# Kernel optimization log

Hardware: AMD Instinct MI355X
Metric: run time of the kernel (lower is better)

The kernel has to match this reference:

```python
import jax, jax.numpy as jnp
import numpy as np

N = 1024
D = 128          # node_dim
NUM_LAYERS = 3
H_CLS = 128      # edge classifier hidden


def setup_inputs() -> dict:
    key = jax.random.key(0)
    ks = jax.random.split(key, 20)
    s_in = 1.0 / np.sqrt(3.0)
    s_d = 1.0 / np.sqrt(D)
    s_2d = 1.0 / np.sqrt(2 * D)
    s_h = 1.0 / np.sqrt(H_CLS)
    inp = {
        "node_features": jax.random.uniform(ks[0], (N, 3), jnp.float32),
        "adj_matrix": jax.random.uniform(ks[1], (N, N), jnp.float32),
        "edge_weights": jax.random.normal(ks[2], (N, N, 1), jnp.float32),
        # node embedding Linear(3, D)
        "W_embed": jax.random.uniform(ks[3], (3, D), jnp.float32, -s_in, s_in),
        "b_embed": jax.random.uniform(ks[4], (D,), jnp.float32, -s_in, s_in),
        # stacked GCN layer params, [L, ...]
        "Wu": jax.random.uniform(ks[5], (NUM_LAYERS, D, D), jnp.float32, -s_d, s_d),
        "bu": jax.random.uniform(ks[6], (NUM_LAYERS, D), jnp.float32, -s_d, s_d),
        "Wv": jax.random.uniform(ks[7], (NUM_LAYERS, D, D), jnp.float32, -s_d, s_d),
        "bv": jax.random.uniform(ks[8], (NUM_LAYERS, D), jnp.float32, -s_d, s_d),
        "Wg": jax.random.uniform(ks[9], (NUM_LAYERS, 2 * D, D), jnp.float32, -s_2d, s_2d),
        "bg": jax.random.uniform(ks[10], (NUM_LAYERS, D), jnp.float32, -s_2d, s_2d),
        # edge classifier: Linear(2D, 128) -> ReLU -> Linear(128, 1)
        "Wc1": jax.random.uniform(ks[11], (2 * D, H_CLS), jnp.float32, -s_2d, s_2d),
        "bc1": jax.random.uniform(ks[12], (H_CLS,), jnp.float32, -s_2d, s_2d),
        "Wc2": jax.random.uniform(ks[13], (H_CLS, 1), jnp.float32, -s_h, s_h),
        "bc2": jax.random.uniform(ks[14], (1,), jnp.float32, -s_h, s_h),
    }
    return inp


def reference(node_features, adj_matrix, edge_weights,
              W_embed, b_embed, Wu, bu, Wv, bv, Wg, bg,
              Wc1, bc1, Wc2, bc2):
    h = node_features @ W_embed + b_embed                       # [N, D]
    for l in range(NUM_LAYERS):
        u = h @ Wu[l] + bu[l]                                   # [N, D]
        v = h @ Wv[l] + bv[l]                                   # [N, D]
        agg = adj_matrix @ v                                    # [N, D]
        # gate Linear(2D, D) on cat([u, agg]) == u @ Wg[:D] + agg @ Wg[D:]
        gate = jax.nn.sigmoid(u @ Wg[l, :D] + agg @ Wg[l, D:] + bg[l])
        h = jax.nn.relu(h + gate * agg)
    # edge classifier: cat([h_i, h_j]) @ Wc1 == (h @ Wc1[:D])[i] + (h @ Wc1[D:])[j]
    hi = h @ Wc1[:D]                                            # [N, H]
    hj = h @ Wc1[D:]                                            # [N, H]
    hidden = jax.nn.relu(hi[:, None, :] + hj[None, :, :] + bc1) # [N, N, H]
    logits = jnp.einsum('ijh,h->ij', hidden, Wc2[:, 0]) + bc2[0]  # [N, N]
    loss = jnp.mean(jnp.square(logits * adj_matrix - edge_weights[..., 0]))
    return logits, loss
```

## Files before the change

kernel.cpp:

```cpp
#include <hip/hip_runtime.h>

#define NN 1024
#define DD 128
#define NBLK 256

typedef __attribute__((ext_vector_type(4))) float f32x4;

__device__ __forceinline__ void scstore(float* p, float v) {
    __hip_atomic_store((unsigned*)p, __float_as_uint(v),
                       __ATOMIC_RELAXED, __HIP_MEMORY_SCOPE_AGENT);
}

__device__ __forceinline__ void gridbar(unsigned* bar, unsigned ep) {
    __syncthreads();
    if (threadIdx.x == 0) {
        asm volatile("s_waitcnt vmcnt(0)" ::: "memory");
        unsigned old = __hip_atomic_fetch_add(&bar[(blockIdx.x & 15) << 5], 1u,
                                              __ATOMIC_RELAXED, __HIP_MEMORY_SCOPE_AGENT);
        if (old == (ep << 4) - 1) {
            unsigned mold = __hip_atomic_fetch_add(&bar[512], 1u,
                                                   __ATOMIC_RELAXED, __HIP_MEMORY_SCOPE_AGENT);
            if (mold == (ep << 4) - 1)
                __hip_atomic_store(&bar[544], ep, __ATOMIC_RELAXED, __HIP_MEMORY_SCOPE_AGENT);
        }
        while (__hip_atomic_load(&bar[544], __ATOMIC_RELAXED, __HIP_MEMORY_SCOPE_AGENT) < ep)
            __builtin_amdgcn_s_sleep(4);
    }
    __syncthreads();
}

__device__ __forceinline__ float dotW2(const float* __restrict__ W, const float* x, int d) {
    float a0 = 0.f, a1 = 0.f;
#pragma unroll 2
    for (int k = 0; k < DD; k += 8) {
        f32x4 xa = *(const f32x4*)(x + k);
        f32x4 xb = *(const f32x4*)(x + k + 4);
        a0 = fmaf(xa[0], W[(k + 0) * DD + d], a0);
        a0 = fmaf(xa[1], W[(k + 1) * DD + d], a0);
        a0 = fmaf(xa[2], W[(k + 2) * DD + d], a0);
        a0 = fmaf(xa[3], W[(k + 3) * DD + d], a0);
        a1 = fmaf(xb[0], W[(k + 4) * DD + d], a1);
        a1 = fmaf(xb[1], W[(k + 5) * DD + d], a1);
        a1 = fmaf(xb[2], W[(k + 6) * DD + d], a1);
        a1 = fmaf(xb[3], W[(k + 7) * DD + d], a1);
    }
    return a0 + a1;
}

__global__ __launch_bounds__(1024, 4) void k_fused(
    const float* __restrict__ adj, const float* __restrict__ ew,
    const float* __restrict__ nf, const float* __restrict__ We, const float* __restrict__ be,
    const float* __restrict__ Wu, const float* __restrict__ bu,
    const float* __restrict__ Wv, const float* __restrict__ bv,
    const float* __restrict__ Wg, const float* __restrict__ bg,
    const float* __restrict__ Wc1, const float* __restrict__ bc1,
    const float* __restrict__ Wc2, const float* __restrict__ bc2,
    float* __restrict__ vA, float* __restrict__ vB, float* __restrict__ vC,
    float* __restrict__ hi, float* __restrict__ hj,
    float* __restrict__ S1, float* __restrict__ S2,
    float* __restrict__ lossAcc, unsigned* __restrict__ counter,
    unsigned* __restrict__ barCnt, float* __restrict__ outL)
{
    __shared__ float hS[4][DD], uS[4][DD], aggS[4][DD];
    __shared__ float gg[2][4][DD];
    __shared__ float sred[2][4][2];
    __shared__ float wS[DD];
    __shared__ union {
        struct { float adjS[4][NN]; float pS[16][4][DD]; } g;
        struct { float hiS[64][132]; float hjS[64][130]; float lred[16]; } e;
    } sm;

    int tid = threadIdx.x, bx = blockIdx.x;
    int row0 = bx * 4;
    int halfq = tid >> 9, rq = (tid >> 7) & 3, d = tid & 127;
    unsigned ep = 0;

    {
        int r = tid >> 8, k0 = (tid & 255) << 2;
        *(f32x4*)&sm.g.adjS[r][k0] = *(const f32x4*)(adj + (size_t)(row0 + r) * NN + k0);
    }
    if (tid < 512) {
        int r = tid >> 7;
        float a = be[d];
#pragma unroll
        for (int k = 0; k < 3; ++k) a = fmaf(nf[(row0 + r) * 3 + k], We[k * DD + d], a);
        hS[r][d] = a;
    }
    __syncthreads();
    {
        float acc = dotW2(halfq ? Wv : Wu, hS[rq], d);
        if (!halfq) uS[rq][d] = acc + bu[d];
        else        scstore(&vA[(size_t)(row0 + rq) * DD + d], acc + bv[d]);
    }
    gridbar(barCnt, ++ep);

    for (int l = 0; l < 3; ++l) {
        const float* vin = (l == 0) ? vA : (l == 1) ? vB : vC;
        float* vout = (l == 0) ? vB : vC;

        {
            int kk = tid >> 5, dq = tid & 31;
            int d0 = dq << 2, kb = kk << 5;
            f32x4 ac0 = {0.f,0.f,0.f,0.f}, ac1 = ac0, ac2 = ac0, ac3 = ac0;
#pragma unroll 2
            for (int ku = 0; ku < 32; ku += 4) {
                f32x4 a0 = *(const f32x4*)&sm.g.adjS[0][kb + ku];
                f32x4 a1 = *(const f32x4*)&sm.g.adjS[1][kb + ku];
                f32x4 a2 = *(const f32x4*)&sm.g.adjS[2][kb + ku];
                f32x4 a3 = *(const f32x4*)&sm.g.adjS[3][kb + ku];
#pragma unroll
                for (int j = 0; j < 4; ++j) {
                    f32x4 v4 = *(const f32x4*)(vin + (size_t)(kb + ku + j) * DD + d0);
#pragma unroll
                    for (int c = 0; c < 4; ++c) {
                        ac0[c] = fmaf(a0[j], v4[c], ac0[c]);
                        ac1[c] = fmaf(a1[j], v4[c], ac1[c]);
                        ac2[c] = fmaf(a2[j], v4[c], ac2[c]);
                        ac3[c] = fmaf(a3[j], v4[c], ac3[c]);
                    }
                }
            }
            if (kk >= 16) {
                int ks = kk - 16;
                *(f32x4*)&sm.g.pS[ks][0][d0] = ac0;
                *(f32x4*)&sm.g.pS[ks][1][d0] = ac1;
                *(f32x4*)&sm.g.pS[ks][2][d0] = ac2;
                *(f32x4*)&sm.g.pS[ks][3][d0] = ac3;
            }
            __syncthreads();
            if (kk < 16) {
                f32x4 p0 = *(const f32x4*)&sm.g.pS[kk][0][d0];
                f32x4 p1 = *(const f32x4*)&sm.g.pS[kk][1][d0];
                f32x4 p2 = *(const f32x4*)&sm.g.pS[kk][2][d0];
                f32x4 p3 = *(const f32x4*)&sm.g.pS[kk][3][d0];
#pragma unroll
                for (int c = 0; c < 4; ++c) {
                    p0[c] += ac0[c]; p1[c] += ac1[c]; p2[c] += ac2[c]; p3[c] += ac3[c];
                }
                *(f32x4*)&sm.g.pS[kk][0][d0] = p0;
                *(f32x4*)&sm.g.pS[kk][1][d0] = p1;
                *(f32x4*)&sm.g.pS[kk][2][d0] = p2;
                *(f32x4*)&sm.g.pS[kk][3][d0] = p3;
            }
        }
        __syncthreads();
        if (tid < 512) {
            int r = tid >> 7;
            float s = 0.f;
#pragma unroll
            for (int c = 0; c < 16; ++c) s += sm.g.pS[c][r][d];
            aggS[r][d] = s;
        }
        __syncthreads();
        {
            const float* W = Wg + l * (2 * DD * DD) + (halfq ? DD * DD : 0);
            gg[halfq][rq][d] = dotW2(W, halfq ? aggS[rq] : uS[rq], d);
        }
        __syncthreads();
        if (tid < 512) {
            int r = tid >> 7;
            float g = 1.f / (1.f + __expf(-(gg[0][r][d] + gg[1][r][d] + bg[l * DD + d])));
            float nh = fmaf(g, aggS[r][d], hS[r][d]);
            hS[r][d] = nh > 0.f ? nh : 0.f;
        }
        __syncthreads();
        {
            const float* W2 = (l < 2) ? ((halfq ? Wv : Wu) + (l + 1) * DD * DD)
                                      : (Wc1 + (halfq ? DD * DD : 0));
            float acc = dotW2(W2, hS[rq], d);
            if (l < 2) {
                if (!halfq) uS[rq][d] = acc + bu[(l + 1) * DD + d];
                else        scstore(&vout[(size_t)(row0 + rq) * DD + d], acc + bv[(l + 1) * DD + d]);
            } else {
                float val = acc + (halfq ? 0.f : bc1[d]);
                scstore(&(halfq ? hj : hi)[(size_t)(row0 + rq) * DD + d], val);
                float p = val * Wc2[d];
#pragma unroll
                for (int off = 32; off; off >>= 1) p += __shfl_down(p, off);
                if ((tid & 63) == 0) sred[halfq][rq][(tid >> 6) & 1] = p;
            }
        }
        if (l == 2) {
            __syncthreads();
            if (tid < 4) scstore(&S1[row0 + tid], sred[0][tid][0] + sred[0][tid][1]);
            else if (tid < 8) scstore(&S2[row0 + tid - 4], sred[1][tid - 4][0] + sred[1][tid - 4][1]);
        }
        gridbar(barCnt, ++ep);
    }

    {
        int i0 = (bx >> 4) << 6, j0 = (bx & 15) << 6;
        if (tid < 128) wS[tid] = Wc2[tid];
        for (int e2 = tid; e2 < 2048; e2 += 1024) {
            int r = e2 >> 5, c = (e2 & 31) << 2;
            *(f32x4*)&sm.e.hiS[r][c] = *(const f32x4*)(hi + (size_t)(i0 + r) * DD + c);
            f32x4 jv = *(const f32x4*)(hj + (size_t)(j0 + r) * DD + c);
            float2 j01; j01.x = jv[0]; j01.y = jv[1];
            float2 j23; j23.x = jv[2]; j23.y = jv[3];
            *(float2*)&sm.e.hjS[r][c] = j01;
            *(float2*)&sm.e.hjS[r][c + 2] = j23;
        }
        __syncthreads();
        int ty = tid >> 5, tx = tid & 31;
        float a00 = 0.f, a01 = 0.f, a10 = 0.f, a11 = 0.f;
#pragma unroll 4
        for (int hh = 0; hh < DD; hh += 4) {
            f32x4 x0 = *(const f32x4*)&sm.e.hiS[ty][hh];
            f32x4 x1 = *(const f32x4*)&sm.e.hiS[ty + 32][hh];
            float2 y0a = *(const float2*)&sm.e.hjS[tx][hh];
            float2 y0b = *(const float2*)&sm.e.hjS[tx][hh + 2];
            float2 y1a = *(const float2*)&sm.e.hjS[tx + 32][hh];
            float2 y1b = *(const float2*)&sm.e.hjS[tx + 32][hh + 2];
            f32x4 w4 = *(const f32x4*)&wS[hh];
            a00 = fmaf(fabsf(x0[0] + y0a.x), w4[0], a00);
            a00 = fmaf(fabsf(x0[1] + y0a.y), w4[1], a00);
            a00 = fmaf(fabsf(x0[2] + y0b.x), w4[2], a00);
            a00 = fmaf(fabsf(x0[3] + y0b.y), w4[3], a00);
            a01 = fmaf(fabsf(x0[0] + y1a.x), w4[0], a01);
            a01 = fmaf(fabsf(x0[1] + y1a.y), w4[1], a01);
            a01 = fmaf(fabsf(x0[2] + y1b.x), w4[2], a01);
            a01 = fmaf(fabsf(x0[3] + y1b.y), w4[3], a01);
            a10 = fmaf(fabsf(x1[0] + y0a.x), w4[0], a10);
            a10 = fmaf(fabsf(x1[1] + y0a.y), w4[1], a10);
            a10 = fmaf(fabsf(x1[2] + y0b.x), w4[2], a10);
            a10 = fmaf(fabsf(x1[3] + y0b.y), w4[3], a10);
            a11 = fmaf(fabsf(x1[0] + y1a.x), w4[0], a11);
            a11 = fmaf(fabsf(x1[1] + y1a.y), w4[1], a11);
            a11 = fmaf(fabsf(x1[2] + y1b.x), w4[2], a11);
            a11 = fmaf(fabsf(x1[3] + y1b.y), w4[3], a11);
        }
        float bcv = bc2[0];
        int ia = i0 + ty, ib = ia + 32, ja = j0 + tx, jb = ja + 32;
        float s1a = S1[ia], s1b = S1[ib];
        float s2a = S2[ja], s2b = S2[jb];
        float lg00 = fmaf(0.5f, a00 + s1a + s2a, bcv);
        float lg01 = fmaf(0.5f, a01 + s1a + s2b, bcv);
        float lg10 = fmaf(0.5f, a10 + s1b + s2a, bcv);
        float lg11 = fmaf(0.5f, a11 + s1b + s2b, bcv);
        size_t o00 = (size_t)ia * NN + ja, o01 = (size_t)ia * NN + jb;
        size_t o10 = (size_t)ib * NN + ja, o11 = (size_t)ib * NN + jb;
        outL[o00] = lg00; outL[o01] = lg01; outL[o10] = lg10; outL[o11] = lg11;
        float t0 = fmaf(lg00, adj[o00], -ew[o00]);
        float t1 = fmaf(lg01, adj[o01], -ew[o01]);
        float t2 = fmaf(lg10, adj[o10], -ew[o10]);
        float t3 = fmaf(lg11, adj[o11], -ew[o11]);
        float ls = fmaf(t0, t0, fmaf(t1, t1, fmaf(t2, t2, t3 * t3)));
#pragma unroll
        for (int off = 32; off; off >>= 1) ls += __shfl_down(ls, off);
        if ((tid & 63) == 0) sm.e.lred[tid >> 6] = ls;
        __syncthreads();
        if (tid == 0) {
            float bls = 0.f;
#pragma unroll
            for (int w = 0; w < 16; ++w) bls += sm.e.lred[w];
            atomicAdd(lossAcc, bls);
            asm volatile("s_waitcnt vmcnt(0)" ::: "memory");
            unsigned old = atomicAdd(counter, 1u);
            if (old == NBLK - 1u) {
                unsigned Lb = __hip_atomic_load((unsigned*)lossAcc,
                                                __ATOMIC_RELAXED, __HIP_MEMORY_SCOPE_AGENT);
                outL[(size_t)NN * NN] = __uint_as_float(Lb) * (1.f / (1024.f * 1024.f));
            }
        }
    }
}

extern "C" void kernel_launch(void* const* d_in, const int* in_sizes, int n_in,
                              void* d_out, int out_size, void* d_ws, size_t ws_size,
                              hipStream_t stream)
{
    const float* nf  = (const float*)d_in[0];
    const float* adj = (const float*)d_in[1];
    const float* ew  = (const float*)d_in[2];
    const float* We  = (const float*)d_in[3];
    const float* be  = (const float*)d_in[4];
    const float* Wu  = (const float*)d_in[5];
    const float* bu  = (const float*)d_in[6];
    const float* Wv  = (const float*)d_in[7];
    const float* bv  = (const float*)d_in[8];
    const float* Wg  = (const float*)d_in[9];
    const float* bg  = (const float*)d_in[10];
    const float* Wc1 = (const float*)d_in[11];
    const float* bc1 = (const float*)d_in[12];
    const float* Wc2 = (const float*)d_in[13];
    const float* bc2 = (const float*)d_in[14];

    float* ws = (float*)d_ws;
    float* vA  = ws;
    float* vB  = ws + 131072;
    float* vC  = ws + 262144;
    float* hi  = ws + 393216;
    float* hj  = ws + 524288;
    float* S1  = ws + 655360;
    float* S2  = ws + 656384;
    float* lossAcc = ws + 657408;
    unsigned* counter = (unsigned*)(ws + 657409);
    unsigned* barCnt = (unsigned*)(ws + 657440);

    hipMemsetAsync((void*)lossAcc, 0, 2560, stream);
    k_fused<<<NBLK, 1024, 0, stream>>>(adj, ew, nf, We, be, Wu, bu, Wv, bv, Wg, bg,
                                       Wc1, bc1, Wc2, bc2, vA, vB, vC, hi, hj, S1, S2,
                                       lossAcc, counter, barCnt, (float*)d_out);
}
```

Before: 172.3 us.

## Overlap gate u-projection with adjacency aggregation via warp specialization

The block is split so the lower 512 threads compute the gate's u @ Wg[:D] product while the upper 512 threads compute the adj @ v aggregation, each covering twice the K range. This removes one barrier and the two-stage partial-sum reduction, and shortens the later gate phase to only the agg half. The cost is that the aggregation now runs on half the threads with longer per-thread loops, so the two halves may be unbalanced.

New measurement: 173.2 us. About the same (+0.5%).

```diff
diff --git a/kernel.cpp b/kernel.cpp
--- a/kernel.cpp
+++ b/kernel.cpp
@@ -98,50 +98,40 @@
         const float* vin = (l == 0) ? vA : (l == 1) ? vB : vC;
         float* vout = (l == 0) ? vB : vC;
 
-        {
-            int kk = tid >> 5, dq = tid & 31;
-            int d0 = dq << 2, kb = kk << 5;
+        if (tid < 512) {
+            const float* WA = Wg + l * (2 * DD * DD);
+            gg[0][rq][d] = dotW2(WA, uS[rq], d);
+        } else {
+            int t = tid - 512;
+            int kk = t >> 5, dq = t & 31;
+            int d0 = dq << 2;
             f32x4 ac0 = {0.f,0.f,0.f,0.f}, ac1 = ac0, ac2 = ac0, ac3 = ac0;
+#pragma unroll
+            for (int cc = 0; cc < 2; ++cc) {
+                int kb = (kk + cc * 16) << 5;
 #pragma unroll 2
-            for (int ku = 0; ku < 32; ku += 4) {
-                f32x4 a0 = *(const f32x4*)&sm.g.adjS[0][kb + ku];
-                f32x4 a1 = *(const f32x4*)&sm.g.adjS[1][kb + ku];
-                f32x4 a2 = *(const f32x4*)&sm.g.adjS[2][kb + ku];
-                f32x4 a3 = *(const f32x4*)&sm.g.adjS[3][kb + ku];
-#pragma unroll
-                for (int j = 0; j < 4; ++j) {
-                    f32x4 v4 = *(const f32x4*)(vin + (size_t)(kb + ku + j) * DD + d0);
-#pragma unroll
-                    for (int c = 0; c < 4; ++c) {
-                        ac0[c] = fmaf(a0[j], v4[c], ac0[c]);
-                        ac1[c] = fmaf(a1[j], v4[c], ac1[c]);
-                        ac2[c] = fmaf(a2[j], v4[c], ac2[c]);
-                        ac3[c] = fmaf(a3[j], v4[c], ac3[c]);
+                for (int ku = 0; ku < 32; ku += 4) {
+                    f32x4 a0 = *(const f32x4*)&sm.g.adjS[0][kb + ku];
+                    f32x4 a1 = *(const f32x4*)&sm.g.adjS[1][kb + ku];
+                    f32x4 a2 = *(const f32x4*)&sm.g.adjS[2][kb + ku];
+                    f32x4 a3 = *(const f32x4*)&sm.g.adjS[3][kb + ku];
+#pragma unroll
+                    for (int j = 0; j < 4; ++j) {
+                        f32x4 v4 = *(const f32x4*)(vin + (size_t)(kb + ku + j) * DD + d0);
+#pragma unroll
+                        for (int c = 0; c < 4; ++c) {
+                            ac0[c] = fmaf(a0[j], v4[c], ac0[c]);
+                            ac1[c] = fmaf(a1[j], v4[c], ac1[c]);
+                            ac2[c] = fmaf(a2[j], v4[c], ac2[c]);
+                            ac3[c] = fmaf(a3[j], v4[c], ac3[c]);
+                        }
                     }
                 }
             }
-            if (kk >= 16) {
-                int ks = kk - 16;
-                *(f32x4*)&sm.g.pS[ks][0][d0] = ac0;
-                *(f32x4*)&sm.g.pS[ks][1][d0] = ac1;
-                *(f32x4*)&sm.g.pS[ks][2][d0] = ac2;
-                *(f32x4*)&sm.g.pS[ks][3][d0] = ac3;
-            }
-            __syncthreads();
-            if (kk < 16) {
-                f32x4 p0 = *(const f32x4*)&sm.g.pS[kk][0][d0];
-                f32x4 p1 = *(const f32x4*)&sm.g.pS[kk][1][d0];
-                f32x4 p2 = *(const f32x4*)&sm.g.pS[kk][2][d0];
-                f32x4 p3 = *(const f32x4*)&sm.g.pS[kk][3][d0];
-#pragma unroll
-                for (int c = 0; c < 4; ++c) {
-                    p0[c] += ac0[c]; p1[c] += ac1[c]; p2[c] += ac2[c]; p3[c] += ac3[c];
-                }
-                *(f32x4*)&sm.g.pS[kk][0][d0] = p0;
-                *(f32x4*)&sm.g.pS[kk][1][d0] = p1;
-                *(f32x4*)&sm.g.pS[kk][2][d0] = p2;
-                *(f32x4*)&sm.g.pS[kk][3][d0] = p3;
-            }
+            *(f32x4*)&sm.g.pS[kk][0][d0] = ac0;
+            *(f32x4*)&sm.g.pS[kk][1][d0] = ac1;
+            *(f32x4*)&sm.g.pS[kk][2][d0] = ac2;
+            *(f32x4*)&sm.g.pS[kk][3][d0] = ac3;
         }
         __syncthreads();
         if (tid < 512) {
@@ -152,9 +142,9 @@
             aggS[r][d] = s;
         }
         __syncthreads();
-        {
-            const float* W = Wg + l * (2 * DD * DD) + (halfq ? DD * DD : 0);
-            gg[halfq][rq][d] = dotW2(W, halfq ? aggS[rq] : uS[rq], d);
+        if (tid < 512) {
+            const float* WB = Wg + l * (2 * DD * DD) + DD * DD;
+            gg[1][rq][d] = dotW2(WB, aggS[rq], d);
         }
         __syncthreads();
         if (tid < 512) {
```
